# Performance work log

Measured on AMD Instinct MI355X. Metric: run time of the kernel, lower is better.

The kernel has to match this reference:

```python
import jax, jax.numpy as jnp
import numpy as np

B, S, H = 4, 2048, 1024

def setup_inputs() -> dict:
    key = jax.random.key(0)
    ks = jax.random.split(key, 7)
    scale = 1.0 / np.sqrt(H)
    x  = jax.random.normal(ks[0], (B, S, H), dtype=jnp.float32)
    Wq = jax.random.normal(ks[1], (H, H), dtype=jnp.float32) * scale
    bq = jax.random.normal(ks[2], (H,), dtype=jnp.float32) * 0.01
    Wk = jax.random.normal(ks[3], (H, H), dtype=jnp.float32) * scale
    bk = jax.random.normal(ks[4], (H,), dtype=jnp.float32) * 0.01
    Wv = jax.random.normal(ks[5], (H, H), dtype=jnp.float32) * scale
    bv = jax.random.normal(ks[6], (H,), dtype=jnp.float32) * 0.01
    return {"x": x, "Wq": Wq, "bq": bq, "Wk": Wk, "bk": bk, "Wv": Wv, "bv": bv}

def reference(x, Wq, bq, Wk, bk, Wv, bv):
    # q/k/v: [B, S, H]
    q = jnp.einsum('bsh,hd->bsd', x, Wq.T) + bq
    k = jnp.einsum('bsh,hd->bsd', x, Wk.T) + bk
    v = jnp.einsum('bsh,hd->bsd', x, Wv.T) + bv
    # NOTE: original module applies NO 1/sqrt(H) scaling.
    scores = jnp.einsum('bqd,bkd->bqk', q, k)  # [B, S, S]
    attn = jax.nn.softmax(scores, axis=-1)
    return jnp.einsum('bqk,bkd->bqd', attn, v)  # [B, S, H]
```

## Files before the change

### kernel.cpp

```cpp
#include <hip/hip_runtime.h>
#include <hip/hip_bf16.h>


typedef __attribute__((ext_vector_type(4))) float f32x4;
typedef __attribute__((ext_vector_type(16))) float f32x16;
typedef __attribute__((ext_vector_type(8))) _Float16 f16x8;
typedef __attribute__((ext_vector_type(4))) unsigned short us4;
typedef __attribute__((ext_vector_type(8))) unsigned short us8;

#define MFMA16F(a, b, c) __builtin_amdgcn_mfma_f32_16x16x32_f16((a), (b), (c), 0, 0, 0)
#define MFMA32F(a, b, c) __builtin_amdgcn_mfma_f32_32x32x16_f16((a), (b), (c), 0, 0, 0)

static __device__ __forceinline__ unsigned short f2h_u(float x) {
  _Float16 h = (_Float16)x;
  return *reinterpret_cast<unsigned short*>(&h);
}
static __device__ __forceinline__ float hu2f(unsigned short u) {
  _Float16 h;
  *reinterpret_cast<unsigned short*>(&h) = u;
  return (float)h;
}

__global__ __launch_bounds__(256) void split_x_kernel(
    const float* __restrict__ in, unsigned short* __restrict__ outp, int ntiles) {
  const int t = blockIdx.x * 256 + threadIdx.x;
  if (t >= ntiles * 64) return;
  const int tile = t >> 6;
  const int l = t & 63;
  const int m = (tile >> 5) * 16 + (l & 15);
  const int kb = (tile & 31) * 32 + (l >> 4) * 8;
  const float* src = in + (size_t)m * 1024 + kb;
  f32x4 v0 = *(const f32x4*)src;
  f32x4 v1 = *(const f32x4*)(src + 4);
  us8 h;
#pragma unroll
  for (int j = 0; j < 4; j++) {
    h[j] = f2h_u(v0[j]);
    h[j + 4] = f2h_u(v1[j]);
  }
  *(us8*)(outp + (size_t)tile * 512 + l * 8) = h;
}

__global__ __launch_bounds__(256) void split3_kernel(
    const float* __restrict__ w0, const float* __restrict__ w1,
    const float* __restrict__ w2,
    unsigned short* __restrict__ h0, unsigned short* __restrict__ l0,
    unsigned short* __restrict__ h1, unsigned short* __restrict__ l1,
    unsigned short* __restrict__ h2, unsigned short* __restrict__ l2) {
  const int which = blockIdx.y;
  const float* in = which == 0 ? w0 : (which == 1 ? w1 : w2);
  unsigned short* hi = which == 0 ? h0 : (which == 1 ? h1 : h2);
  unsigned short* lo = which == 0 ? l0 : (which == 1 ? l1 : l2);
  const int t = blockIdx.x * 256 + threadIdx.x;
  const int tile = t >> 6;
  const int l = t & 63;
  const int m = (tile >> 5) * 16 + (l & 15);
  const int kb = (tile & 31) * 32 + (l >> 4) * 8;
  const float* src = in + (size_t)m * 1024 + kb;
  f32x4 v0 = *(const f32x4*)src;
  f32x4 v1 = *(const f32x4*)(src + 4);
  us8 h, lv;
#pragma unroll
  for (int j = 0; j < 4; j++) {
    unsigned short hu = f2h_u(v0[j]);
    h[j] = hu;
    lv[j] = f2h_u(v0[j] - hu2f(hu));
    hu = f2h_u(v1[j]);
    h[j + 4] = hu;
    lv[j + 4] = f2h_u(v1[j] - hu2f(hu));
  }
  *(us8*)(hi + (size_t)tile * 512 + l * 8) = h;
  if (which != 2) *(us8*)(lo + (size_t)tile * 512 + l * 8) = lv;
}

__global__ __launch_bounds__(256, 2) void proj_fused_kernel(
    const unsigned short* __restrict__ Xf,
    const unsigned short* __restrict__ Wqh, const unsigned short* __restrict__ Wql,
    const unsigned short* __restrict__ Wkh, const unsigned short* __restrict__ Wkl,
    const unsigned short* __restrict__ Wvh,
    const float* __restrict__ bq, const float* __restrict__ bk,
    const float* __restrict__ bv,
    unsigned short* __restrict__ Qf, unsigned short* __restrict__ Kf,
    unsigned short* __restrict__ Vt) {
  const int tid = threadIdx.x;
  const int lane = tid & 63;
  const int wid = tid >> 6;
  const int lrow = lane & 15;
  const int kg = lane >> 4;
  const int bx = blockIdx.x;
  const int ntb = blockIdx.y * 16 + wid * 4;
  const int z = blockIdx.z;

  const unsigned short* Wh = z == 0 ? Wqh : (z == 1 ? Wkh : Wvh);
  const unsigned short* Wl = z == 0 ? Wql : Wkl;
  const float* bias = z == 0 ? bq : (z == 1 ? bk : bv);

  const unsigned short* xf = Xf + (size_t)(bx * 8) * 32 * 512 + lane * 8;

  f32x4 acc[8][4];
#pragma unroll
  for (int mf = 0; mf < 8; mf++)
#pragma unroll
    for (int cf = 0; cf < 4; cf++) acc[mf][cf] = f32x4{0.f, 0.f, 0.f, 0.f};

  if (z < 2) {
    for (int kt = 0; kt < 32; kt++) {
      const size_t o = (size_t)kt * 512;
      f16x8 ah[8];
#pragma unroll
      for (int mf = 0; mf < 8; mf++)
        ah[mf] = *(const f16x8*)(xf + (size_t)mf * 32 * 512 + o);
#pragma unroll
      for (int cf = 0; cf < 4; cf++) {
        const size_t wo = ((size_t)(ntb + cf) * 32 + kt) * 512 + lane * 8;
        f16x8 bh = *(const f16x8*)(Wh + wo);
        f16x8 bl = *(const f16x8*)(Wl + wo);
#pragma unroll
        for (int mf = 0; mf < 8; mf++) {
          acc[mf][cf] = MFMA16F(ah[mf], bh, acc[mf][cf]);
          acc[mf][cf] = MFMA16F(ah[mf], bl, acc[mf][cf]);
        }
      }
    }
    unsigned short* O = z == 0 ? Qf : Kf;
    const int b = bx >> 4;
#pragma unroll
    for (int mf = 0; mf < 8; mf++) {
      const int s0 = (bx & 15) * 128 + mf * 16 + kg * 4;
#pragma unroll
      for (int cf = 0; cf < 4; cf++) {
        const int nt = ntb + cf;
        const float bv_ = bias[nt * 16 + lrow];
#pragma unroll
        for (int i = 0; i < 4; i++) {
          const int s = s0 + i;
          const size_t a = ((size_t)((b * 64 + (s >> 5)) * 64 + nt)) * 512 +
                           (s & 31) * 16 + lrow;
          O[a] = f2h_u(acc[mf][cf][i] + bv_);
        }
      }
    }
  } else {
    for (int kt = 0; kt < 32; kt++) {
      const size_t o = (size_t)kt * 512;
      f16x8 ah[8];
#pragma unroll
      for (int mf = 0; mf < 8; mf++)
        ah[mf] = *(const f16x8*)(xf + (size_t)mf * 32 * 512 + o);
#pragma unroll
      for (int cf = 0; cf < 4; cf++) {
        const size_t wo = ((size_t)(ntb + cf) * 32 + kt) * 512 + lane * 8;
        f16x8 bh = *(const f16x8*)(Wh + wo);
#pragma unroll
        for (int mf = 0; mf < 8; mf++) acc[mf][cf] = MFMA16F(ah[mf], bh, acc[mf][cf]);
      }
    }
    const int b = bx >> 4;
#pragma unroll
    for (int mf = 0; mf < 8; mf++) {
      const int kl_hi = (bx & 15) * 8 + mf;
#pragma unroll
      for (int cf = 0; cf < 4; cf++) {
        const int d = (ntb + cf) * 16 + lrow;
        const float bv_ = bias[d];
        us4 pk;
#pragma unroll
        for (int i = 0; i < 4; i++) pk[i] = f2h_u(acc[mf][cf][i] + bv_);
        const size_t a = ((size_t)(b * 32 + (d >> 5)) * 128 + kl_hi) * 512 +
                         (size_t)(d & 31) * 16 + kg * 4;
        *reinterpret_cast<us4*>(&Vt[a]) = pk;
      }
    }
  }
}

__global__ __launch_bounds__(1024, 1) void attn_part_kernel(
    const unsigned short* __restrict__ Qf, const unsigned short* __restrict__ Kf,
    const unsigned short* __restrict__ Vt, unsigned short* __restrict__ Opart,
    float* __restrict__ Mpart, float* __restrict__ Lpart) {
  __shared__ unsigned short LDSB[65536];
  __shared__ float redM[16][64];
  __shared__ float redS[16][64];

  const int tid = threadIdx.x;
  const int lane = tid & 63;
  const int wid = tid >> 6;
  const int lq = lane & 31;
  const int hi = lane >> 5;
  const int lo16 = lq * 16 + hi * 8;

  const int id = blockIdx.x;
  const int xcd = id & 7;
  const int b = xcd >> 1;
  const int kh = xcd & 1;
  const int qt = id >> 3;

  {
    const us8* qsrc = (const us8*)(Qf + ((size_t)(b * 64 + qt * 2) * 64) * 512);
    us8* qdst = (us8*)LDSB;
#pragma unroll
    for (int i = 0; i < 8; i++) {
      const int u = i * 1024 + tid;
      const int kk = u >> 7, rem = u & 127;
      qdst[u] = qsrc[(rem >> 6) * 4096 + kk * 64 + (rem & 63)];
    }
  }
  __syncthreads();

  f32x16 s00, s01, s10, s11;
#pragma unroll
  for (int r = 0; r < 16; r++) { s00[r] = 0.f; s01[r] = 0.f; s10[r] = 0.f; s11[r] = 0.f; }

  const unsigned short* kb =
      Kf + ((size_t)(b * 64 + kh * 32 + wid * 2) * 64) * 512 + lo16;
#define KLD(G, KKK) (*(const f16x8*)(kb + (size_t)(G)*64 * 512 + (size_t)(KKK)*512))
  f16x8 kc0 = KLD(0, 0), kc1 = KLD(1, 0);
  for (int kk = 0; kk < 63; kk++) {
    f16x8 qA = *(const f16x8*)&LDSB[kk * 1024 + lo16];
    f16x8 qB = *(const f16x8*)&LDSB[kk * 1024 + 512 + lo16];
    f16x8 kn0 = KLD(0, kk + 1), kn1 = KLD(1, kk + 1);
    __builtin_amdgcn_s_setprio(1);
    s00 = MFMA32F(kc0, qA, s00);
    s01 = MFMA32F(kc0, qB, s01);
    s10 = MFMA32F(kc1, qA, s10);
    s11 = MFMA32F(kc1, qB, s11);
    __builtin_amdgcn_s_setprio(0);
    kc0 = kn0; kc1 = kn1;
  }
  {
    f16x8 qA = *(const f16x8*)&LDSB[63 * 1024 + lo16];
    f16x8 qB = *(const f16x8*)&LDSB[63 * 1024 + 512 + lo16];
    s00 = MFMA32F(kc0, qA, s00);
    s01 = MFMA32F(kc0, qB, s01);
    s10 = MFMA32F(kc1, qA, s10);
    s11 = MFMA32F(kc1, qB, s11);
  }
#undef KLD

  float mA = -3.0e38f, mB = -3.0e38f;
#pragma unroll
  for (int r = 0; r < 16; r++) {
    mA = fmaxf(mA, fmaxf(s00[r], s10[r]));
    mB = fmaxf(mB, fmaxf(s01[r], s11[r]));
  }
  mA = fmaxf(mA, __shfl_xor(mA, 32));
  mB = fmaxf(mB, __shfl_xor(mB, 32));
  if (hi == 0) { redM[wid][lq] = mA; redM[wid][32 + lq] = mB; }
  __syncthreads();
  float MA = redM[0][lq], MB = redM[0][32 + lq];
#pragma unroll
  for (int w = 1; w < 16; w++) {
    MA = fmaxf(MA, redM[w][lq]);
    MB = fmaxf(MB, redM[w][32 + lq]);
  }
  float sA = 0.f, sB = 0.f;
#pragma unroll
  for (int r = 0; r < 16; r++) {
    s00[r] = __expf(s00[r] - MA); sA += s00[r];
    s10[r] = __expf(s10[r] - MA); sA += s10[r];
    s01[r] = __expf(s01[r] - MB); sB += s01[r];
    s11[r] = __expf(s11[r] - MB); sB += s11[r];
  }
  sA += __shfl_xor(sA, 32);
  sB += __shfl_xor(sB, 32);
  if (hi == 0) { redS[wid][lq] = sA; redS[wid][32 + lq] = sB; }

  const int swz = (lq & 7) << 3;
#define PW(ACC, QQ, KB)                                                       \
  {                                                                           \
    _Pragma("unroll")                                                         \
    for (int qd = 0; qd < 4; qd++) {                                          \
      us4 pk;                                                                 \
      _Pragma("unroll")                                                       \
      for (int i = 0; i < 4; i++) pk[i] = f2h_u(ACC[qd * 4 + i]);             \
      *(us4*)&LDSB[(((QQ)*1024) + (KB) + qd * 8 + 4 * hi) ^ swz] = pk;        \
    }                                                                         \
  }
  PW(s00, lq, wid * 64)
  PW(s01, 32 + lq, wid * 64)
  PW(s10, lq, wid * 64 + 32)
  PW(s11, 32 + lq, wid * 64 + 32)
#undef PW
  __syncthreads();

  if (tid < 64) {
    float M = redM[0][tid], L = redS[0][tid];
#pragma unroll
    for (int w = 1; w < 16; w++) {
      M = fmaxf(M, redM[w][tid]);
      L += redS[w][tid];
    }
    const size_t gi = (size_t)(b * 2 + kh) * 2048 + qt * 64 + tid;
    Mpart[gi] = M;
    Lpart[gi] = L;
  }

  f32x16 o00, o01, o10, o11;
#pragma unroll
  for (int r = 0; r < 16; r++) { o00[r] = 0.f; o01[r] = 0.f; o10[r] = 0.f; o11[r] = 0.f; }

  const unsigned short* vb =
      Vt + ((size_t)((b * 32 + wid * 2) * 128) + kh * 64) * 512 + lo16;
#define VLD(G, KKK) (*(const f16x8*)(vb + (size_t)(G)*128 * 512 + (size_t)(KKK)*512))
  f16x8 vc0 = VLD(0, 0), vc1 = VLD(1, 0);
  const int prA = lq * 1024 + hi * 8;
  const int prB = (32 + lq) * 1024 + hi * 8;
  for (int kk = 0; kk < 63; kk++) {
    f16x8 paA = *(const f16x8*)&LDSB[(prA + kk * 16) ^ swz];
    f16x8 paB = *(const f16x8*)&LDSB[(prB + kk * 16) ^ swz];
    f16x8 vn0 = VLD(0, kk + 1), vn1 = VLD(1, kk + 1);
    __builtin_amdgcn_s_setprio(1);
    o00 = MFMA32F(paA, vc0, o00);
    o01 = MFMA32F(paA, vc1, o01);
    o10 = MFMA32F(paB, vc0, o10);
    o11 = MFMA32F(paB, vc1, o11);
    __builtin_amdgcn_s_setprio(0);
    vc0 = vn0; vc1 = vn1;
  }
  {
    f16x8 paA = *(const f16x8*)&LDSB[(prA + 63 * 16) ^ swz];
    f16x8 paB = *(const f16x8*)&LDSB[(prB + 63 * 16) ^ swz];
    o00 = MFMA32F(paA, vc0, o00);
    o01 = MFMA32F(paA, vc1, o01);
    o10 = MFMA32F(paB, vc0, o10);
    o11 = MFMA32F(paB, vc1, o11);
  }
#undef VLD

  unsigned short* ob = Opart + ((size_t)(b * 2 + kh) * 2048 + qt * 64) * 1024;
  const int d0 = wid * 64 + lq;
#pragma unroll
  for (int r = 0; r < 16; r++) {
    const int crow = (r & 3) + 8 * (r >> 2) + 4 * hi;
    ob[(size_t)crow * 1024 + d0] = f2h_u(o00[r]);
    ob[(size_t)crow * 1024 + d0 + 32] = f2h_u(o01[r]);
    ob[(size_t)(crow + 32) * 1024 + d0] = f2h_u(o10[r]);
    ob[(size_t)(crow + 32) * 1024 + d0 + 32] = f2h_u(o11[r]);
  }
}

__global__ __launch_bounds__(256) void attn_combine_kernel(
    const unsigned short* __restrict__ Opart, const float* __restrict__ Mpart,
    const float* __restrict__ Lpart, float* __restrict__ out) {
  const int t = blockIdx.x * 256 + threadIdx.x;
  const int row = t >> 7;
  const int dd = (t & 127) * 8;
  const int b = row >> 11, sl = row & 2047;
  const int i0 = (b * 2) * 2048 + sl, i1 = i0 + 2048;
  const float m0 = Mpart[i0], m1 = Mpart[i1];
  const float M = fmaxf(m0, m1);
  float w0 = __expf(m0 - M), w1 = __expf(m1 - M);
  const float inv = 1.0f / (w0 * Lpart[i0] + w1 * Lpart[i1]);
  w0 *= inv; w1 *= inv;
  const us8 o0 = *(const us8*)&Opart[(size_t)i0 * 1024 + dd];
  const us8 o1 = *(const us8*)&Opart[(size_t)i1 * 1024 + dd];
  float* op = out + (size_t)row * 1024 + dd;
  f32x4 r0, r1;
#pragma unroll
  for (int j = 0; j < 4; j++) {
    r0[j] = w0 * hu2f(o0[j]) + w1 * hu2f(o1[j]);
    r1[j] = w0 * hu2f(o0[j + 4]) + w1 * hu2f(o1[j + 4]);
  }
  *(f32x4*)op = r0;
  *(f32x4*)(op + 4) = r1;
}

extern "C" void kernel_launch(void* const* d_in, const int* in_sizes, int n_in,
                              void* d_out, int out_size, void* d_ws, size_t ws_size,
                              hipStream_t stream) {
  const float* x  = (const float*)d_in[0];
  const float* Wq = (const float*)d_in[1];
  const float* bq = (const float*)d_in[2];
  const float* Wk = (const float*)d_in[3];
  const float* bk = (const float*)d_in[4];
  const float* Wv = (const float*)d_in[5];
  const float* bv = (const float*)d_in[6];
  float* o = (float*)d_out;

  const size_t NX = (size_t)8192 * 1024;
  const size_t NW = (size_t)1024 * 1024;
  unsigned short* p = (unsigned short*)d_ws;
  unsigned short* Xf = p; p += NX;
  unsigned short* Qf = p; p += NX;
  unsigned short* Kf = p; p += NX;
  unsigned short* Vt = p; p += NX;
  unsigned short* Wqh = p; p += NW;
  unsigned short* Wql = p; p += NW;
  unsigned short* Wkh = p; p += NW;
  unsigned short* Wkl = p; p += NW;
  unsigned short* Wvh = p; p += NW;
  unsigned short* Wvl = p; p += NW;
  unsigned short* Opart = p; p += 2 * NX;
  float* Mpart = (float*)p; p += 32768;
  float* Lpart = (float*)p; p += 32768;

  split_x_kernel<<<4096, 256, 0, stream>>>(x, Xf, 16384);
  dim3 gs(512, 3);
  split3_kernel<<<gs, 256, 0, stream>>>(Wq, Wk, Wv, Wqh, Wql, Wkh, Wkl, Wvh, Wvl);

  dim3 gp(64, 4, 3), bp(256);
  proj_fused_kernel<<<gp, bp, 0, stream>>>(Xf, Wqh, Wql, Wkh, Wkl, Wvh,
                                           bq, bk, bv, Qf, Kf, Vt);

  attn_part_kernel<<<256, 1024, 0, stream>>>(Qf, Kf, Vt, Opart, Mpart, Lpart);
  attn_combine_kernel<<<4096, 256, 0, stream>>>(Opart, Mpart, Lpart, o);
}
```

Before: 183.9 us.

## Stage X tiles through double-buffered LDS in projection kernel

The projection kernel now copies each chunk of the X operand into a double-buffered 128KB shared-memory tile cooperatively, then reads MFMA A-fragments from LDS instead of each wave loading them from global memory. This is meant to cut redundant global/L2 traffic, since all four waves in the block previously fetched the same X fragments. The large LDS allocation forces one block per CU, so launch bounds drop from 2 to 1 block per SM. That lowers occupancy and adds a barrier per chunk.

```diff
diff --git a/kernel.cpp b/kernel.cpp
--- a/kernel.cpp
+++ b/kernel.cpp
@@ -73,7 +73,7 @@
   if (which != 2) *(us8*)(lo + (size_t)tile * 512 + l * 8) = lv;
 }
 
-__global__ __launch_bounds__(256, 2) void proj_fused_kernel(
+__global__ __launch_bounds__(256, 1) void proj_fused_kernel(
     const unsigned short* __restrict__ Xf,
     const unsigned short* __restrict__ Wqh, const unsigned short* __restrict__ Wql,
     const unsigned short* __restrict__ Wkh, const unsigned short* __restrict__ Wkl,
@@ -82,6 +82,8 @@
     const float* __restrict__ bv,
     unsigned short* __restrict__ Qf, unsigned short* __restrict__ Kf,
     unsigned short* __restrict__ Vt) {
+  __shared__ unsigned short XS[2 * 32768];
+
   const int tid = threadIdx.x;
   const int lane = tid & 63;
   const int wid = tid >> 6;
@@ -95,7 +97,20 @@
   const unsigned short* Wl = z == 0 ? Wql : Wkl;
   const float* bias = z == 0 ? bq : (z == 1 ? bk : bv);
 
-  const unsigned short* xf = Xf + (size_t)(bx * 8) * 32 * 512 + lane * 8;
+  const us8* xsrc = (const us8*)(Xf + (size_t)(bx * 8) * 32 * 512);
+
+#define STAGE(C, BUF)                                                         \
+  {                                                                           \
+    us8* dst = (us8*)&XS[(BUF)*32768];                                        \
+    _Pragma("unroll 4")                                                       \
+    for (int j = 0; j < 16; j++) {                                            \
+      const int flat = j * 256 + tid;                                         \
+      const int mf_ = flat >> 9;                                              \
+      const int ktl_ = (flat >> 6) & 7;                                       \
+      const int e_ = flat & 63;                                               \
+      dst[flat] = xsrc[((size_t)mf_ * 32 + (C)*8 + ktl_) * 64 + e_];          \
+    }                                                                         \
+  }
 
   f32x4 acc[8][4];
 #pragma unroll
@@ -103,24 +118,33 @@
 #pragma unroll
     for (int cf = 0; cf < 4; cf++) acc[mf][cf] = f32x4{0.f, 0.f, 0.f, 0.f};
 
+  STAGE(0, 0)
+  __syncthreads();
+
   if (z < 2) {
-    for (int kt = 0; kt < 32; kt++) {
-      const size_t o = (size_t)kt * 512;
-      f16x8 ah[8];
-#pragma unroll
-      for (int mf = 0; mf < 8; mf++)
-        ah[mf] = *(const f16x8*)(xf + (size_t)mf * 32 * 512 + o);
-#pragma unroll
-      for (int cf = 0; cf < 4; cf++) {
-        const size_t wo = ((size_t)(ntb + cf) * 32 + kt) * 512 + lane * 8;
-        f16x8 bh = *(const f16x8*)(Wh + wo);
-        f16x8 bl = *(const f16x8*)(Wl + wo);
-#pragma unroll
-        for (int mf = 0; mf < 8; mf++) {
-          acc[mf][cf] = MFMA16F(ah[mf], bh, acc[mf][cf]);
-          acc[mf][cf] = MFMA16F(ah[mf], bl, acc[mf][cf]);
+    for (int c = 0; c < 4; c++) {
+      if (c < 3) STAGE(c + 1, (c + 1) & 1)
+      const unsigned short* xs = &XS[(c & 1) * 32768];
+#pragma unroll 2
+      for (int ktl = 0; ktl < 8; ktl++) {
+        const int kt = c * 8 + ktl;
+        f16x8 ah[8];
+#pragma unroll
+        for (int mf = 0; mf < 8; mf++)
+          ah[mf] = *(const f16x8*)(xs + (mf * 8 + ktl) * 512 + lane * 8);
+#pragma unroll
+        for (int cf = 0; cf < 4; cf++) {
+          const size_t wo = ((size_t)(ntb + cf) * 32 + kt) * 512 + lane * 8;
+          f16x8 bh = *(const f16x8*)(Wh + wo);
+          f16x8 bl = *(const f16x8*)(Wl + wo);
+#pragma unroll
+          for (int mf = 0; mf < 8; mf++) {
+            acc[mf][cf] = MFMA16F(ah[mf], bh, acc[mf][cf]);
+            acc[mf][cf] = MFMA16F(ah[mf], bl, acc[mf][cf]);
+          }
         }
       }
+      __syncthreads();
     }
     unsigned short* O = z == 0 ? Qf : Kf;
     const int b = bx >> 4;
@@ -141,19 +165,26 @@
       }
     }
   } else {
-    for (int kt = 0; kt < 32; kt++) {
-      const size_t o = (size_t)kt * 512;
-      f16x8 ah[8];
-#pragma unroll
-      for (int mf = 0; mf < 8; mf++)
-        ah[mf] = *(const f16x8*)(xf + (size_t)mf * 32 * 512 + o);
-#pragma unroll
-      for (int cf = 0; cf < 4; cf++) {
-        const size_t wo = ((size_t)(ntb + cf) * 32 + kt) * 512 + lane * 8;
-        f16x8 bh = *(const f16x8*)(Wh + wo);
-#pragma unroll
-        for (int mf = 0; mf < 8; mf++) acc[mf][cf] = MFMA16F(ah[mf], bh, acc[mf][cf]);
+    for (int c = 0; c < 4; c++) {
+      if (c < 3) STAGE(c + 1, (c + 1) & 1)
+      const unsigned short* xs = &XS[(c & 1) * 32768];
+#pragma unroll 2
+      for (int ktl = 0; ktl < 8; ktl++) {
+        const int kt = c * 8 + ktl;
+        f16x8 ah[8];
+#pragma unroll
+        for (int mf = 0; mf < 8; mf++)
+          ah[mf] = *(const f16x8*)(xs + (mf * 8 + ktl) * 512 + lane * 8);
+#pragma unroll
+        for (int cf = 0; cf < 4; cf++) {
+          const size_t wo = ((size_t)(ntb + cf) * 32 + kt) * 512 + lane * 8;
+          f16x8 bh = *(const f16x8*)(Wh + wo);
+#pragma unroll
+          for (int mf = 0; mf < 8; mf++)
+            acc[mf][cf] = MFMA16F(ah[mf], bh, acc[mf][cf]);
+        }
       }
+      __syncthreads();
     }
     const int b = bx >> 4;
 #pragma unroll
@@ -172,6 +203,7 @@
       }
     }
   }
+#undef STAGE
 }
 
 __global__ __launch_bounds__(1024, 1) void attn_part_kernel(
```

Result: slower. 239.4 us (+30.1%).
